# Kernel tuning notes

Hardware: AMD Instinct MI355X
Metric: run time of the kernel (lower is better)

Reference implementation:

```python
import jax, jax.numpy as jnp
import numpy as np

T, B, I, H, O = 2048, 128, 32, 128, 1


def setup_inputs() -> dict:
    key = jax.random.key(0)
    ks = jax.random.split(key, 5)
    X = jax.random.normal(ks[0], (T, B, I), dtype=jnp.float32)
    W_in = jax.random.normal(ks[1], (H, I), dtype=jnp.float32) / np.sqrt(I)
    W_hh = jax.random.normal(ks[2], (H, H), dtype=jnp.float32) / np.sqrt(H)
    rnn_bias = jnp.zeros((H,), dtype=jnp.float32)
    alpha = jax.random.uniform(ks[3], (H,), dtype=jnp.float32)
    value_W = jax.random.normal(ks[4], (O, H), dtype=jnp.float32) / np.sqrt(H)
    value_bias = jnp.zeros((O,), dtype=jnp.float32)
    return {"X": X, "W_in": W_in, "W_hh": W_hh, "rnn_bias": rnn_bias,
            "alpha": alpha, "value_W": value_W, "value_bias": value_bias}


def reference(X, W_in, W_hh, rnn_bias, alpha, value_W, value_bias):
    # X: (T, B, I). Precompute input projections for all timesteps at once.
    xproj = jnp.einsum('tbi,hi->tbh', X, W_in)  # (T, B, H)

    def step(h_prev, xp_t):
        h_tilde = jnp.tanh(xp_t + h_prev @ W_hh.T + rnn_bias)
        h = (1.0 - alpha) * h_prev + alpha * h_tilde  # per-unit leaky blend
        return h, h

    h0 = jnp.zeros((X.shape[1], W_hh.shape[0]), dtype=X.dtype)
    last_hidden, Z = jax.lax.scan(step, h0, xproj)  # Z: (T, B, H)
    V = value_bias + jnp.einsum('tbh,oh->tbo', Z, value_W)  # (T, B, O)
    return V, last_hidden
```

## Files before the change

### kernel.cpp

```cpp
#include <hip/hip_runtime.h>

#define TT 2048
#define BB 128
#define II 32
#define HH 128
#define NW (TT / 8)

typedef float v2f __attribute__((ext_vector_type(2)));
typedef float v4f __attribute__((ext_vector_type(4)));
typedef unsigned int u32;
typedef __attribute__((address_space(3))) u32 lds_u32;
typedef const __attribute__((address_space(1))) u32 glb_u32;

__device__ __forceinline__ v2f pk_fma(v2f a, v2f b, v2f c) {
    v2f d;
    asm("v_pk_fma_f32 %0, %1, %2, %3" : "=v"(d) : "v"(a), "v"(b), "v"(c));
    return d;
}

template <int CTRL>
__device__ __forceinline__ float dpp_mov(float p) {
    return __int_as_float(__builtin_amdgcn_update_dpp(0, __float_as_int(p), CTRL, 0xF, 0xF, true));
}
template <int CTRL>
__device__ __forceinline__ float dpp_add(float p) {
    return p + dpp_mov<CTRL>(p);
}
template <int CTRL>
__device__ __forceinline__ float pair_red(float x, float y, bool sel) {
    float keep = sel ? y : x;
    float give = sel ? x : y;
    return keep + dpp_mov<CTRL>(give);
}

__global__ __launch_bounds__(256)
void vrnn_kernel(const float* __restrict__ X, const float* __restrict__ W_in,
                 const float* __restrict__ W_hh, const float* __restrict__ rnn_bias,
                 const float* __restrict__ alpha, const float* __restrict__ value_W,
                 const float* __restrict__ value_bias, float* __restrict__ out)
{
    const int b    = blockIdx.x;
    const int tid  = threadIdx.x;
    const int wave = tid >> 6;
    const int lane = tid & 63;
    const int g    = lane >> 4;
    const int j    = lane & 15;
    const int base = 32 * wave + 8 * g;
    const int rown = base + (j & 7);

    __shared__ __align__(16) float xw[2][8][II];
    __shared__ __align__(16) float hbuf[2][192];

    if (wave == 0) {
        const float* src = X + (size_t)(lane >> 3) * (BB * II) + b * II + (lane & 7) * 4;
        __builtin_amdgcn_global_load_lds((glb_u32*)src, (lds_u32*)(&xw[0][0][0]), 16, 0, 0);
    }

    v2f wh[8][4], wi8[8], binit[8];
#pragma unroll
    for (int r = 0; r < 8; ++r) {
        const float* wr = W_hh + (size_t)(base + r) * HH + 8 * j;
        v4f a0 = *(const v4f*)(wr);
        v4f a1 = *(const v4f*)(wr + 4);
        wh[r][0] = (v2f){a0.x, a0.y}; wh[r][1] = (v2f){a0.z, a0.w};
        wh[r][2] = (v2f){a1.x, a1.y}; wh[r][3] = (v2f){a1.z, a1.w};
        wi8[r]   = *(const v2f*)(W_in + (size_t)(base + r) * II + 2 * j);
        binit[r] = (v2f){ (j == 0) ? rnn_bias[base + r] : 0.0f, 0.0f };
    }
    v2f vwc[4];
#pragma unroll
    for (int i = 0; i < 4; ++i) vwc[i] = *(const v2f*)(value_W + 8 * j + 2 * i);
    const float al_own = alpha[rown];
    const float vb     = value_bias[0];
    const bool  b0 = (j & 1) != 0;
    const bool  b1 = (j & 2) != 0;
    const bool  b2 = (j & 4) != 0;
    const int   woff = 12 * (4 * wave + g) + (j & 7);
    float hreg = 0.0f;

    if (tid < 192) hbuf[1][tid] = 0.0f;
    __syncthreads();

    float* outV = out;
    float* outH = out + (size_t)TT * BB;

    for (int w = 0; w < NW; ++w) {
        if (wave == 0 && w + 1 < NW) {
            const float* src = X + (size_t)((w + 1) * 8 + (lane >> 3)) * (BB * II)
                                 + b * II + (lane & 7) * 4;
            __builtin_amdgcn_global_load_lds((glb_u32*)src,
                (lds_u32*)(&xw[(w + 1) & 1][0][0]), 16, 0, 0);
        }
#pragma unroll
        for (int s = 0; s < 8; ++s) {
            const int par = s & 1;
            const float* hb = &hbuf[par ^ 1][12 * j];
            const v4f h0 = *(const v4f*)(hb);
            const v4f h1 = *(const v4f*)(hb + 4);
            v2f hp[4] = { (v2f){h0.x, h0.y}, (v2f){h0.z, h0.w},
                          (v2f){h1.x, h1.y}, (v2f){h1.z, h1.w} };
            const v2f xc = *(const v2f*)(&xw[w & 1][s][2 * j]);
            float p[8];
#pragma unroll
            for (int r = 0; r < 8; ++r) {
                v2f a = pk_fma(wi8[r], xc, binit[r]);
                a = pk_fma(wh[r][0], hp[0], a);
                a = pk_fma(wh[r][1], hp[1], a);
                a = pk_fma(wh[r][2], hp[2], a);
                a = pk_fma(wh[r][3], hp[3], a);
                p[r] = a.x + a.y;
            }
            float q0 = pair_red<0xB1>(p[0], p[1], b0);
            float q1 = pair_red<0xB1>(p[2], p[3], b0);
            float q2 = pair_red<0xB1>(p[4], p[5], b0);
            float q3 = pair_red<0xB1>(p[6], p[7], b0);
            float r0 = pair_red<0x4E>(q0, q1, b1);
            float r1 = pair_red<0x4E>(q2, q3, b1);
            const float k3  = b2 ? r1 : r0;
            const float g3  = b2 ? r0 : r1;
            const float vL  = dpp_mov<0x104>(g3);
            const float vR  = dpp_mov<0x114>(g3);
            float pre = k3 + (b2 ? vR : vL);
            pre += dpp_mov<0x128>(pre);
            const float e  = __builtin_amdgcn_exp2f(pre * 2.8853900817779268f);
            const float rc = __builtin_amdgcn_rcpf(e + 1.0f);
            const float gt = fmaf(-2.0f, rc, 1.0f);
            hreg = fmaf(al_own, gt - hreg, hreg);
            hbuf[par][woff] = hreg;
            if (wave == (s & 3)) {
                if ((w | s) != 0) {
                    v2f vt = vwc[0] * hp[0];
                    vt = pk_fma(vwc[1], hp[1], vt);
                    vt = pk_fma(vwc[2], hp[2], vt);
                    vt = pk_fma(vwc[3], hp[3], vt);
                    float vs = vt.x + vt.y;
                    vs = dpp_add<0xB1>(vs);
                    vs = dpp_add<0x4E>(vs);
                    const float uL = dpp_mov<0x104>(vs);
                    const float uR = dpp_mov<0x114>(vs);
                    vs += b2 ? uR : uL;
                    vs = dpp_add<0x128>(vs);
                    if (lane == 0)
                        outV[(size_t)(8 * w + s - 1) * BB + b] = vb + vs;
                }
            }
            if (wave == 0 && s == 7)
                asm volatile("s_waitcnt vmcnt(0)" ::: "memory");
            asm volatile("s_waitcnt lgkmcnt(0)" ::: "memory");
            __builtin_amdgcn_s_barrier();
        }
    }

    if (wave == 0) {
        const float* hb = &hbuf[1][12 * j];
        const v4f h0 = *(const v4f*)(hb);
        const v4f h1 = *(const v4f*)(hb + 4);
        v2f hp[4] = { (v2f){h0.x, h0.y}, (v2f){h0.z, h0.w},
                      (v2f){h1.x, h1.y}, (v2f){h1.z, h1.w} };
        v2f vt = vwc[0] * hp[0];
        vt = pk_fma(vwc[1], hp[1], vt);
        vt = pk_fma(vwc[2], hp[2], vt);
        vt = pk_fma(vwc[3], hp[3], vt);
        float vs = vt.x + vt.y;
        vs = dpp_add<0xB1>(vs);
        vs = dpp_add<0x4E>(vs);
        const float uL = dpp_mov<0x104>(vs);
        const float uR = dpp_mov<0x114>(vs);
        vs += b2 ? uR : uL;
        vs = dpp_add<0x128>(vs);
        if (lane == 0)
            outV[(size_t)(TT - 1) * BB + b] = vb + vs;
    }
    if (j < 8)
        outH[(size_t)b * HH + base + j] = hreg;
}

extern "C" void kernel_launch(void* const* d_in, const int* in_sizes, int n_in,
                              void* d_out, int out_size, void* d_ws, size_t ws_size,
                              hipStream_t stream) {
    const float* X      = (const float*)d_in[0];
    const float* W_in   = (const float*)d_in[1];
    const float* W_hh   = (const float*)d_in[2];
    const float* rbias  = (const float*)d_in[3];
    const float* alpha  = (const float*)d_in[4];
    const float* vW     = (const float*)d_in[5];
    const float* vbias  = (const float*)d_in[6];
    float* out = (float*)d_out;

    vrnn_kernel<<<dim3(BB), dim3(256), 0, stream>>>(X, W_in, W_hh, rbias, alpha, vW, vbias, out);
}
```

Before: 792.8 us.

## Prescale weights for tanh, defer value head off critical path, buffer outputs in LDS

New measurement: 807.4 us. Within noise of the previous version (+1.8%).

```diff
diff --git a/kernel.cpp b/kernel.cpp
--- a/kernel.cpp
+++ b/kernel.cpp
@@ -50,11 +50,14 @@
 
     __shared__ __align__(16) float xw[2][8][II];
     __shared__ __align__(16) float hbuf[2][192];
+    __shared__ __align__(16) float vres[TT];
 
     if (wave == 0) {
         const float* src = X + (size_t)(lane >> 3) * (BB * II) + b * II + (lane & 7) * 4;
         __builtin_amdgcn_global_load_lds((glb_u32*)src, (lds_u32*)(&xw[0][0][0]), 16, 0, 0);
     }
+
+    const float SC = 2.8853900817779268f;
 
     v2f wh[8][4], wi8[8], binit[8];
 #pragma unroll
@@ -62,10 +65,11 @@
         const float* wr = W_hh + (size_t)(base + r) * HH + 8 * j;
         v4f a0 = *(const v4f*)(wr);
         v4f a1 = *(const v4f*)(wr + 4);
-        wh[r][0] = (v2f){a0.x, a0.y}; wh[r][1] = (v2f){a0.z, a0.w};
-        wh[r][2] = (v2f){a1.x, a1.y}; wh[r][3] = (v2f){a1.z, a1.w};
-        wi8[r]   = *(const v2f*)(W_in + (size_t)(base + r) * II + 2 * j);
-        binit[r] = (v2f){ (j == 0) ? rnn_bias[base + r] : 0.0f, 0.0f };
+        wh[r][0] = (v2f){a0.x * SC, a0.y * SC}; wh[r][1] = (v2f){a0.z * SC, a0.w * SC};
+        wh[r][2] = (v2f){a1.x * SC, a1.y * SC}; wh[r][3] = (v2f){a1.z * SC, a1.w * SC};
+        v2f wiv  = *(const v2f*)(W_in + (size_t)(base + r) * II + 2 * j);
+        wi8[r]   = (v2f){wiv.x * SC, wiv.y * SC};
+        binit[r] = (v2f){ (j == 0) ? rnn_bias[base + r] * SC : 0.0f, 0.0f };
     }
     v2f vwc[4];
 #pragma unroll
@@ -77,6 +81,8 @@
     const bool  b2 = (j & 4) != 0;
     const int   woff = 12 * (4 * wave + g) + (j & 7);
     float hreg = 0.0f;
+    float hpre = 0.0f;
+    v2f hpPrev[4] = { (v2f){0,0}, (v2f){0,0}, (v2f){0,0}, (v2f){0,0} };
 
     if (tid < 192) hbuf[1][tid] = 0.0f;
     __syncthreads();
@@ -94,12 +100,27 @@
 #pragma unroll
         for (int s = 0; s < 8; ++s) {
             const int par = s & 1;
+            const int t   = 8 * w + s;
             const float* hb = &hbuf[par ^ 1][12 * j];
             const v4f h0 = *(const v4f*)(hb);
             const v4f h1 = *(const v4f*)(hb + 4);
+            const v2f xc = *(const v2f*)(&xw[w & 1][s][2 * j]);
+            if (wave == ((s + 2) & 3) && t >= 2) {
+                v2f vt = vwc[0] * hpPrev[0];
+                vt = pk_fma(vwc[1], hpPrev[1], vt);
+                vt = pk_fma(vwc[2], hpPrev[2], vt);
+                vt = pk_fma(vwc[3], hpPrev[3], vt);
+                float vs = vt.x + vt.y;
+                vs = dpp_add<0xB1>(vs);
+                vs = dpp_add<0x4E>(vs);
+                const float uL = dpp_mov<0x104>(vs);
+                const float uR = dpp_mov<0x114>(vs);
+                vs += b2 ? uR : uL;
+                vs = dpp_add<0x128>(vs);
+                if (lane == 0) vres[t - 2] = vb + vs;
+            }
             v2f hp[4] = { (v2f){h0.x, h0.y}, (v2f){h0.z, h0.w},
                           (v2f){h1.x, h1.y}, (v2f){h1.z, h1.w} };
-            const v2f xc = *(const v2f*)(&xw[w & 1][s][2 * j]);
             float p[8];
 #pragma unroll
             for (int r = 0; r < 8; ++r) {
@@ -122,28 +143,14 @@
             const float vR  = dpp_mov<0x114>(g3);
             float pre = k3 + (b2 ? vR : vL);
             pre += dpp_mov<0x128>(pre);
-            const float e  = __builtin_amdgcn_exp2f(pre * 2.8853900817779268f);
+            const float e  = __builtin_amdgcn_exp2f(pre);
             const float rc = __builtin_amdgcn_rcpf(e + 1.0f);
             const float gt = fmaf(-2.0f, rc, 1.0f);
-            hreg = fmaf(al_own, gt - hreg, hreg);
+            hreg = fmaf(al_own, gt, hpre);
             hbuf[par][woff] = hreg;
-            if (wave == (s & 3)) {
-                if ((w | s) != 0) {
-                    v2f vt = vwc[0] * hp[0];
-                    vt = pk_fma(vwc[1], hp[1], vt);
-                    vt = pk_fma(vwc[2], hp[2], vt);
-                    vt = pk_fma(vwc[3], hp[3], vt);
-                    float vs = vt.x + vt.y;
-                    vs = dpp_add<0xB1>(vs);
-                    vs = dpp_add<0x4E>(vs);
-                    const float uL = dpp_mov<0x104>(vs);
-                    const float uR = dpp_mov<0x114>(vs);
-                    vs += b2 ? uR : uL;
-                    vs = dpp_add<0x128>(vs);
-                    if (lane == 0)
-                        outV[(size_t)(8 * w + s - 1) * BB + b] = vb + vs;
-                }
-            }
+            hpre = fmaf(-al_own, hreg, hreg);
+            hpPrev[0] = hp[0]; hpPrev[1] = hp[1];
+            hpPrev[2] = hp[2]; hpPrev[3] = hp[3];
             if (wave == 0 && s == 7)
                 asm volatile("s_waitcnt vmcnt(0)" ::: "memory");
             asm volatile("s_waitcnt lgkmcnt(0)" ::: "memory");
@@ -152,6 +159,20 @@
     }
 
     if (wave == 0) {
+        v2f vt = vwc[0] * hpPrev[0];
+        vt = pk_fma(vwc[1], hpPrev[1], vt);
+        vt = pk_fma(vwc[2], hpPrev[2], vt);
+        vt = pk_fma(vwc[3], hpPrev[3], vt);
+        float vs = vt.x + vt.y;
+        vs = dpp_add<0xB1>(vs);
+        vs = dpp_add<0x4E>(vs);
+        float uL = dpp_mov<0x104>(vs);
+        float uR = dpp_mov<0x114>(vs);
+        vs += b2 ? uR : uL;
+        vs = dpp_add<0x128>(vs);
+        if (lane == 0) vres[TT - 2] = vb + vs;
+    }
+    if (wave == 1) {
         const float* hb = &hbuf[1][12 * j];
         const v4f h0 = *(const v4f*)(hb);
         const v4f h1 = *(const v4f*)(hb + 4);
@@ -164,15 +185,18 @@
         float vs = vt.x + vt.y;
         vs = dpp_add<0xB1>(vs);
         vs = dpp_add<0x4E>(vs);
-        const float uL = dpp_mov<0x104>(vs);
-        const float uR = dpp_mov<0x114>(vs);
+        float uL = dpp_mov<0x104>(vs);
+        float uR = dpp_mov<0x114>(vs);
         vs += b2 ? uR : uL;
         vs = dpp_add<0x128>(vs);
-        if (lane == 0)
-            outV[(size_t)(TT - 1) * BB + b] = vb + vs;
+        if (lane == 0) vres[TT - 1] = vb + vs;
     }
     if (j < 8)
         outH[(size_t)b * HH + base + j] = hreg;
+    __syncthreads();
+#pragma unroll
+    for (int i = 0; i < TT / 256; ++i)
+        outV[(size_t)(i * 256 + tid) * BB + b] = vres[i * 256 + tid];
 }
 
 extern "C" void kernel_launch(void* const* d_in, const int* in_sizes, int n_in,
```
